# Optimization experiments

Measured on AMD Instinct MI355X. Metric: run time of the kernel, lower is better.

The kernel has to match this reference:

```python
import jax, jax.numpy as jnp
import numpy as np

# ---- Cl(4,1) Cayley table (signature [1,1,1,1,-1]), basis blades indexed by 5-bit mask ----
_METRIC = np.array([1, 1, 1, 1, -1], dtype=np.float32)

def _build_gp_map():
    T = np.zeros((32, 32, 32), dtype=np.float32)
    for a in range(32):
        for b in range(32):
            # canonical reordering sign (count generator swaps)
            s, aa = 0, a >> 1
            while aa:
                s += bin(aa & b).count('1')
                aa >>= 1
            sign = -1.0 if (s & 1) else 1.0
            # metric contribution of annihilated common generators
            common = a & b
            for i in range(5):
                if (common >> i) & 1:
                    sign *= _METRIC[i]
            T[a, b, a ^ b] = sign  # e_a * e_b = sign * e_{a XOR b}
    return T

GP_MAP = _build_gp_map()  # [32, 32, 32], one signed nonzero per (a,b) pair

IN_FEATURES = 256
OUT_FEATURES = 256
BATCH, SEQ = 4, 512


def setup_inputs() -> dict:
    key = jax.random.key(0)
    kx, kw = jax.random.split(key)
    x = jax.random.normal(kx, (BATCH, SEQ, IN_FEATURES, 32), dtype=jnp.float32)
    # Versor init: std = sqrt(2 / (fan_in * 32))
    std = (2.0 / (IN_FEATURES * 32)) ** 0.5
    weight = jax.random.normal(kw, (OUT_FEATURES, IN_FEATURES, 32), dtype=jnp.float32) * std
    return {"x": x, "weight": weight}


def normalize_cl41(out, eps=1e-6):
    # Normalize each output multivector by its Euclidean norm over the 32 basis coeffs.
    norm = jnp.sqrt(jnp.sum(out * out, axis=-1, keepdims=True) + eps)
    return out / norm


def reference(x, weight):
    gp = jnp.asarray(GP_MAP, dtype=x.dtype)  # [j, l, k]
    # W_op[o,i,l,k] = sum_j weight[o,i,j] * gp[j,l,k]
    W_op = jnp.einsum('oij,jlk->oilk', weight, gp)
    # out[b,s,o,k] = sum_{i,l} x[b,s,i,l] * W_op[o,i,l,k]
    out = jnp.einsum('bsil,oilk->bsok', x, W_op)
    return normalize_cl41(out)
```

## Files before the change

### kernel.cpp

```cpp
#include <hip/hip_runtime.h>
#include <stdint.h>

#define AS1 __attribute__((address_space(1)))
#define AS3 __attribute__((address_space(3)))

typedef __attribute__((ext_vector_type(8))) short bf16x8;
typedef __attribute__((ext_vector_type(4))) float f32x4;


struct Mono { int col[4]; int ph[4]; };

constexpr Mono mono_mul(Mono A, Mono B) {
    Mono R{};
    for (int r = 0; r < 4; ++r) {
        int k = A.col[r];
        R.col[r] = B.col[k];
        R.ph[r] = (A.ph[r] + B.ph[k]) & 3;
    }
    return R;
}

constexpr Mono gen(int g) {
    Mono E{};
    for (int r = 0; r < 4; ++r) {
        int r1 = (r >> 1) & 1, r0 = r & 1;
        if (g == 0)      { E.col[r] = r ^ 2; E.ph[r] = 0; }
        else if (g == 1) { E.col[r] = r ^ 2; E.ph[r] = r1 ? 1 : 3; }
        else if (g == 2) { E.col[r] = r ^ 1; E.ph[r] = r1 ? 2 : 0; }
        else if (g == 3) { E.col[r] = r ^ 1; E.ph[r] = ((r1 ? 2 : 0) + (r0 ? 1 : 3)) & 3; }
        else             { E.col[r] = r;     E.ph[r] = (1 + (r1 ? 2 : 0) + (r0 ? 2 : 0)) & 3; }
    }
    return E;
}

struct Blades { Mono m[32]; };
constexpr Blades make_blades() {
    Blades B{};
    for (int A = 0; A < 32; ++A) {
        Mono M{};
        for (int r = 0; r < 4; ++r) { M.col[r] = r; M.ph[r] = 0; }
        for (int g = 0; g < 5; ++g)
            if ((A >> g) & 1) M = mono_mul(M, gen(g));
        B.m[A] = M;
    }
    return B;
}
constexpr Blades BL = make_blades();

struct FwdTab { int bl[4][4][2][4]; float sg[4][4][2][4]; };
constexpr FwdTab make_fwd() {
    FwdTab T{};
    int cnt[4][4][2] = {};
    for (int A = 0; A < 32; ++A)
        for (int r = 0; r < 4; ++r) {
            int c = BL.m[A].col[r], p = BL.m[A].ph[r];
            int rc = p & 1;
            int& n = cnt[r][c][rc];
            T.bl[r][c][rc][n] = A;
            T.sg[r][c][rc][n] = (p & 2) ? -1.f : 1.f;
            ++n;
        }
    return T;
}
constexpr FwdTab FT = make_fwd();

__device__ inline unsigned short f2bf(float f) {
    uint32_t u = __float_as_uint(f);
    u += 0x7FFFu + ((u >> 16) & 1u);
    return (unsigned short)(u >> 16);
}

__global__ __launch_bounds__(256) void xform_kernel(const float* __restrict__ x,
                                                    const float* __restrict__ w,
                                                    unsigned short* __restrict__ Xb,
                                                    unsigned short* __restrict__ Wr) {
    if (blockIdx.x < 2048) {
        int t = blockIdx.x * 256 + threadIdx.x;
        int i = t & 255, n = t >> 8;
        float v[32];
        const float4* xp = (const float4*)(x + (size_t)t * 32);
#pragma unroll
        for (int q = 0; q < 8; ++q) {
            float4 f = xp[q];
            v[q * 4 + 0] = f.x; v[q * 4 + 1] = f.y; v[q * 4 + 2] = f.z; v[q * 4 + 3] = f.w;
        }
#pragma unroll
        for (int b = 0; b < 4; ++b) {
            union { unsigned short s[8]; uint4 u; } r;
#pragma unroll
            for (int c = 0; c < 4; ++c)
#pragma unroll
                for (int rc = 0; rc < 2; ++rc) {
                    float s = 0.f;
#pragma unroll
                    for (int j = 0; j < 4; ++j)
                        s += FT.sg[c][b][rc][j] * v[FT.bl[c][b][rc][j]];
                    r.s[c * 2 + rc] = f2bf(s);
                }
            *((uint4*)(Xb + (size_t)(n * 4 + b) * 2048 + i * 8)) = r.u;
        }
    } else {
        int t = (blockIdx.x - 2048) * 256 + threadIdx.x;
        int i = t & 255, o = t >> 8;
        float v[32];
        const float4* wp = (const float4*)(w + (size_t)t * 32);
#pragma unroll
        for (int q = 0; q < 8; ++q) {
            float4 f = wp[q];
            v[q * 4 + 0] = f.x; v[q * 4 + 1] = f.y; v[q * 4 + 2] = f.z; v[q * 4 + 3] = f.w;
        }
        float Re[4][4], Im[4][4];
#pragma unroll
        for (int a = 0; a < 4; ++a)
#pragma unroll
            for (int c = 0; c < 4; ++c) {
                float sr = 0.f, si = 0.f;
#pragma unroll
                for (int j = 0; j < 4; ++j) {
                    sr += FT.sg[a][c][0][j] * v[FT.bl[a][c][0][j]];
                    si += FT.sg[a][c][1][j] * v[FT.bl[a][c][1][j]];
                }
                Re[a][c] = sr; Im[a][c] = si;
            }
#pragma unroll
        for (int ra = 0; ra < 2; ++ra)
#pragma unroll
            for (int a = 0; a < 4; ++a) {
                int m = o * 8 + ra * 4 + a;
                union { unsigned short s[8]; uint4 u; } r;
#pragma unroll
                for (int c = 0; c < 4; ++c) {
                    float v0 = ra == 0 ? Re[a][c] : Im[a][c];
                    float v1 = ra == 0 ? -Im[a][c] : Re[a][c];
                    r.s[c * 2 + 0] = f2bf(v0);
                    r.s[c * 2 + 1] = f2bf(v1);
                }
                *((uint4*)(Wr + (size_t)m * 2048 + i * 8)) = r.u;
            }
    }
}

__global__ __launch_bounds__(256) void gemm_kernel(const unsigned short* __restrict__ A,
                                                   const unsigned short* __restrict__ B,
                                                   float* __restrict__ out) {
    const int K = 2048;
    __shared__ alignas(16) unsigned short SMEM[2 * 128 * 32];
    unsigned short* As = SMEM;
    unsigned short* Bs = SMEM + 128 * 32;
    float* scr = (float*)SMEM;

    int tid = threadIdx.x;
    int wid = tid >> 6, lane = tid & 63;
    int row0 = blockIdx.y * 128;
    int col0 = blockIdx.x * 128;
    int wr = (wid >> 1) * 64, wc = (wid & 1) * 64;
    int lm = lane & 15, quad = lane >> 4;

    f32x4 acc[4][4];
#pragma unroll
    for (int ti = 0; ti < 4; ++ti)
#pragma unroll
        for (int tj = 0; tj < 4; ++tj)
            acc[ti][tj] = (f32x4){0.f, 0.f, 0.f, 0.f};

    for (int k0 = 0; k0 < K; k0 += 32) {
#pragma unroll
        for (int p = 0; p < 2; ++p) {
            int c = p * 256 + tid;
            int m = c >> 2;
            int off = (c & 3) * 8;
            const unsigned short* ga = A + (size_t)(row0 + m) * K + k0 + off;
            const unsigned short* gb = B + (size_t)(col0 + m) * K + k0 + off;
            unsigned short* la = &As[(size_t)(p * 256 + wid * 64) * 8];
            unsigned short* lb = &Bs[(size_t)(p * 256 + wid * 64) * 8];
            __builtin_amdgcn_global_load_lds((const AS1 void*)ga, (AS3 void*)la, 16, 0, 0);
            __builtin_amdgcn_global_load_lds((const AS1 void*)gb, (AS3 void*)lb, 16, 0, 0);
        }
        __syncthreads();

        bf16x8 af[4], bfr[4];
#pragma unroll
        for (int ti = 0; ti < 4; ++ti)
            af[ti] = *(const bf16x8*)&As[(wr + ti * 16 + lm) * 32 + quad * 8];
#pragma unroll
        for (int tj = 0; tj < 4; ++tj)
            bfr[tj] = *(const bf16x8*)&Bs[(wc + tj * 16 + lm) * 32 + quad * 8];
#pragma unroll
        for (int ti = 0; ti < 4; ++ti)
#pragma unroll
            for (int tj = 0; tj < 4; ++tj)
                acc[ti][tj] = __builtin_amdgcn_mfma_f32_16x16x32_bf16(af[ti], bfr[tj],
                                                                      acc[ti][tj], 0, 0, 0);
        __syncthreads();
    }

    int band = wr >> 6;
#pragma unroll
    for (int ti = 0; ti < 4; ++ti) {
        __syncthreads();
#pragma unroll
        for (int tj = 0; tj < 4; ++tj)
#pragma unroll
            for (int r = 0; r < 4; ++r)
                scr[(band * 16 + quad * 4 + r) * 128 + (wc + tj * 16 + lm)] = acc[ti][tj][r];
        __syncthreads();

        if (tid < 128) {
            int n_l = tid & 31, og = tid >> 5;
            int o_local = (og >> 1) * 8 + ti * 2 + (og & 1);
            int srow0 = (og >> 1) * 16 + (og & 1) * 8;
            float V[32];
#pragma unroll
            for (int u = 0; u < 8; ++u) {
                float4 f = *(const float4*)&scr[(srow0 + u) * 128 + n_l * 4];
                int vi = (u >> 2) * 16 + (u & 3) * 4;
                V[vi + 0] = f.x; V[vi + 1] = f.y; V[vi + 2] = f.z; V[vi + 3] = f.w;
            }
            float xa[32];
            float ss = 0.f;
#pragma unroll
            for (int Ab = 0; Ab < 32; ++Ab) {
                float s = 0.f;
#pragma unroll
                for (int a = 0; a < 4; ++a) {
                    const int c = BL.m[Ab].col[a];
                    const int p = BL.m[Ab].ph[a];
                    float vv = V[(p & 1) * 16 + a * 4 + c];
                    s += (p & 2) ? -vv : vv;
                }
                s *= 0.25f;
                xa[Ab] = s;
                ss += s * s;
            }
            float inv = rsqrtf(ss + 1e-6f);
            int n = (col0 >> 2) + n_l;
            int o = (row0 >> 3) + o_local;
            float4* op = (float4*)(out + ((size_t)n * 256 + o) * 32);
#pragma unroll
            for (int q = 0; q < 8; ++q) {
                float4 f;
                f.x = xa[q * 4 + 0] * inv; f.y = xa[q * 4 + 1] * inv;
                f.z = xa[q * 4 + 2] * inv; f.w = xa[q * 4 + 3] * inv;
                op[q] = f;
            }
        }
    }
}

extern "C" void kernel_launch(void* const* d_in, const int* in_sizes, int n_in,
                              void* d_out, int out_size, void* d_ws, size_t ws_size,
                              hipStream_t stream) {
    const float* x = (const float*)d_in[0];
    const float* w = (const float*)d_in[1];
    float* out = (float*)d_out;

    unsigned short* Wr = (unsigned short*)d_ws;
    unsigned short* Xb = (unsigned short*)((char*)d_ws + 8388608);

    hipLaunchKernelGGL(xform_kernel, dim3(2304),   dim3(256), 0, stream, x, w, Xb, Wr);
    hipLaunchKernelGGL(gemm_kernel,  dim3(64, 16), dim3(256), 0, stream, Wr, Xb, out);
}
```

Baseline: 233.0 us.

## Rewrite GEMM with 256x256 tiles, 4-stage LDS pipeline, and swizzled LDS

Reworks the bf16 MFMA GEMM. It now uses 512-thread blocks computing 256x256 tiles, and a four-buffer LDS ring fed by global_load_lds with three tiles in flight, synchronized by explicit vmcnt waits and barriers. This replaces the previous load, sync, compute, sync loop. It also XOR-swizzles the LDS layout to avoid bank conflicts, raises wave priority around the MFMA bursts, and has each wave run the Clifford epilogue and normalization on its own scratch region, removing the block-wide epilogue barriers. The costs are 128KB of LDS, which limits occupancy, and heavy accumulator register pressure; the grid shrinks to 256 blocks.

```diff
diff --git a/kernel.cpp b/kernel.cpp
--- a/kernel.cpp
+++ b/kernel.cpp
@@ -140,110 +140,141 @@
     }
 }
 
-__global__ __launch_bounds__(256) void gemm_kernel(const unsigned short* __restrict__ A,
-                                                   const unsigned short* __restrict__ B,
-                                                   float* __restrict__ out) {
+__global__ __launch_bounds__(512, 2) void gemm_kernel(const unsigned short* __restrict__ A,
+                                                      const unsigned short* __restrict__ B,
+                                                      float* __restrict__ out) {
     const int K = 2048;
-    __shared__ alignas(16) unsigned short SMEM[2 * 128 * 32];
-    unsigned short* As = SMEM;
-    unsigned short* Bs = SMEM + 128 * 32;
-    float* scr = (float*)SMEM;
-
-    int tid = threadIdx.x;
-    int wid = tid >> 6, lane = tid & 63;
-    int row0 = blockIdx.y * 128;
-    int col0 = blockIdx.x * 128;
-    int wr = (wid >> 1) * 64, wc = (wid & 1) * 64;
-    int lm = lane & 15, quad = lane >> 4;
-
-    f32x4 acc[4][4];
-#pragma unroll
-    for (int ti = 0; ti < 4; ++ti)
-#pragma unroll
-        for (int tj = 0; tj < 4; ++tj)
-            acc[ti][tj] = (f32x4){0.f, 0.f, 0.f, 0.f};
-
-    for (int k0 = 0; k0 < K; k0 += 32) {
+    const int NT = 64;
+    __shared__ alignas(16) unsigned short SM[4 * 16384];
+
+    const int tid = threadIdx.x;
+    const int wid = tid >> 6, lane = tid & 63;
+    const int lm = lane & 15, quad = lane >> 4;
+    const int wm = wid >> 2, wn = wid & 3;
+    const int row0 = blockIdx.y * 256;
+    const int col0 = blockIdx.x * 256;
+
+    size_t gA[2], gB[2];
+    int ldsA[2], ldsB[2];
+#pragma unroll
+    for (int p = 0; p < 2; ++p) {
+        int g = p * 512 + tid;
+        int r = g >> 2, c = g & 3;
+        int sc = c ^ ((r >> 1) & 3);
+        gA[p] = (size_t)(row0 + r) * K + sc * 8;
+        gB[p] = (size_t)(col0 + r) * K + sc * 8;
+        ldsA[p] = (p * 512 + wid * 64) * 8;
+        ldsB[p] = 8192 + (p * 512 + wid * 64) * 8;
+    }
+
+    const int swz = (lm >> 1) & 3;
+    const int aoff = (wm * 128 + lm) * 32 + (quad ^ swz) * 8;
+    const int boff = 8192 + (wn * 64 + lm) * 32 + (quad ^ swz) * 8;
+
+    f32x4 acc[8][4];
+#pragma unroll
+    for (int i = 0; i < 8; ++i)
+#pragma unroll
+        for (int j = 0; j < 4; ++j) acc[i][j] = (f32x4){0.f, 0.f, 0.f, 0.f};
+
+    auto ISSUE = [&](int t) {
+        const int bb = (t & 3) * 16384;
+        const int k0 = t * 32;
 #pragma unroll
         for (int p = 0; p < 2; ++p) {
-            int c = p * 256 + tid;
-            int m = c >> 2;
-            int off = (c & 3) * 8;
-            const unsigned short* ga = A + (size_t)(row0 + m) * K + k0 + off;
-            const unsigned short* gb = B + (size_t)(col0 + m) * K + k0 + off;
-            unsigned short* la = &As[(size_t)(p * 256 + wid * 64) * 8];
-            unsigned short* lb = &Bs[(size_t)(p * 256 + wid * 64) * 8];
-            __builtin_amdgcn_global_load_lds((const AS1 void*)ga, (AS3 void*)la, 16, 0, 0);
-            __builtin_amdgcn_global_load_lds((const AS1 void*)gb, (AS3 void*)lb, 16, 0, 0);
-        }
-        __syncthreads();
-
-        bf16x8 af[4], bfr[4];
-#pragma unroll
-        for (int ti = 0; ti < 4; ++ti)
-            af[ti] = *(const bf16x8*)&As[(wr + ti * 16 + lm) * 32 + quad * 8];
-#pragma unroll
-        for (int tj = 0; tj < 4; ++tj)
-            bfr[tj] = *(const bf16x8*)&Bs[(wc + tj * 16 + lm) * 32 + quad * 8];
-#pragma unroll
-        for (int ti = 0; ti < 4; ++ti)
-#pragma unroll
-            for (int tj = 0; tj < 4; ++tj)
-                acc[ti][tj] = __builtin_amdgcn_mfma_f32_16x16x32_bf16(af[ti], bfr[tj],
-                                                                      acc[ti][tj], 0, 0, 0);
-        __syncthreads();
-    }
-
-    int band = wr >> 6;
-#pragma unroll
-    for (int ti = 0; ti < 4; ++ti) {
-        __syncthreads();
-#pragma unroll
-        for (int tj = 0; tj < 4; ++tj)
-#pragma unroll
-            for (int r = 0; r < 4; ++r)
-                scr[(band * 16 + quad * 4 + r) * 128 + (wc + tj * 16 + lm)] = acc[ti][tj][r];
-        __syncthreads();
-
-        if (tid < 128) {
-            int n_l = tid & 31, og = tid >> 5;
-            int o_local = (og >> 1) * 8 + ti * 2 + (og & 1);
-            int srow0 = (og >> 1) * 16 + (og & 1) * 8;
-            float V[32];
-#pragma unroll
-            for (int u = 0; u < 8; ++u) {
-                float4 f = *(const float4*)&scr[(srow0 + u) * 128 + n_l * 4];
-                int vi = (u >> 2) * 16 + (u & 3) * 4;
-                V[vi + 0] = f.x; V[vi + 1] = f.y; V[vi + 2] = f.z; V[vi + 3] = f.w;
+            __builtin_amdgcn_global_load_lds((const AS1 void*)(A + gA[p] + k0),
+                                             (AS3 void*)(&SM[bb + ldsA[p]]), 16, 0, 0);
+            __builtin_amdgcn_global_load_lds((const AS1 void*)(B + gB[p] + k0),
+                                             (AS3 void*)(&SM[bb + ldsB[p]]), 16, 0, 0);
+        }
+    };
+    auto COMPUTE = [&](int t) {
+        const int bb = (t & 3) * 16384;
+        bf16x8 av[8], bv[4];
+#pragma unroll
+        for (int fn = 0; fn < 4; ++fn) bv[fn] = *(const bf16x8*)&SM[bb + boff + fn * 512];
+#pragma unroll
+        for (int fm = 0; fm < 8; ++fm) av[fm] = *(const bf16x8*)&SM[bb + aoff + fm * 512];
+        __builtin_amdgcn_s_setprio(1);
+#pragma unroll
+        for (int fm = 0; fm < 8; ++fm)
+#pragma unroll
+            for (int fn = 0; fn < 4; ++fn)
+                acc[fm][fn] = __builtin_amdgcn_mfma_f32_16x16x32_bf16(av[fm], bv[fn],
+                                                                      acc[fm][fn], 0, 0, 0);
+        __builtin_amdgcn_s_setprio(0);
+    };
+
+    ISSUE(0); ISSUE(1); ISSUE(2);
+    for (int t = 0; t < NT - 3; ++t) {
+        asm volatile("s_waitcnt vmcnt(8)" ::: "memory");
+        __builtin_amdgcn_s_barrier();
+        ISSUE(t + 3);
+        COMPUTE(t);
+    }
+    asm volatile("s_waitcnt vmcnt(8)" ::: "memory");
+    __builtin_amdgcn_s_barrier();
+    COMPUTE(NT - 3);
+    asm volatile("s_waitcnt vmcnt(4)" ::: "memory");
+    __builtin_amdgcn_s_barrier();
+    COMPUTE(NT - 2);
+    asm volatile("s_waitcnt vmcnt(0)" ::: "memory");
+    __builtin_amdgcn_s_barrier();
+    COMPUTE(NT - 1);
+    __syncthreads();
+
+    float* scrw = (float*)SM + wid * 2048;
+    const int nl = lane >> 2, ol = lane & 3;
+#pragma unroll
+    for (int s = 0; s < 4; ++s) {
+#pragma unroll
+        for (int h = 0; h < 2; ++h)
+#pragma unroll
+            for (int fn = 0; fn < 4; ++fn)
+#pragma unroll
+                for (int r = 0; r < 4; ++r) {
+                    int rw = h * 16 + quad * 4 + r;
+                    int cc = (fn * 16 + lm) ^ (quad << 3);
+                    scrw[rw * 64 + cc] = acc[s * 2 + h][fn][r];
+                }
+        asm volatile("s_waitcnt lgkmcnt(0)" ::: "memory");
+        float V[32];
+#pragma unroll
+        for (int u = 0; u < 8; ++u) {
+            int row = ol * 8 + u;
+            int cb = (nl * 4) ^ (((row >> 2) & 3) << 3);
+            float4 f = *(const float4*)&scrw[row * 64 + cb];
+            int vi = (u >> 2) * 16 + (u & 3) * 4;
+            V[vi + 0] = f.x; V[vi + 1] = f.y; V[vi + 2] = f.z; V[vi + 3] = f.w;
+        }
+        float xa[32];
+        float ss = 0.f;
+#pragma unroll
+        for (int Ab = 0; Ab < 32; ++Ab) {
+            float sv = 0.f;
+#pragma unroll
+            for (int a = 0; a < 4; ++a) {
+                const int c = BL.m[Ab].col[a];
+                const int p = BL.m[Ab].ph[a];
+                float vv = V[(p & 1) * 16 + a * 4 + c];
+                sv += (p & 2) ? -vv : vv;
             }
-            float xa[32];
-            float ss = 0.f;
-#pragma unroll
-            for (int Ab = 0; Ab < 32; ++Ab) {
-                float s = 0.f;
-#pragma unroll
-                for (int a = 0; a < 4; ++a) {
-                    const int c = BL.m[Ab].col[a];
-                    const int p = BL.m[Ab].ph[a];
-                    float vv = V[(p & 1) * 16 + a * 4 + c];
-                    s += (p & 2) ? -vv : vv;
-                }
-                s *= 0.25f;
-                xa[Ab] = s;
-                ss += s * s;
-            }
-            float inv = rsqrtf(ss + 1e-6f);
-            int n = (col0 >> 2) + n_l;
-            int o = (row0 >> 3) + o_local;
-            float4* op = (float4*)(out + ((size_t)n * 256 + o) * 32);
-#pragma unroll
-            for (int q = 0; q < 8; ++q) {
-                float4 f;
-                f.x = xa[q * 4 + 0] * inv; f.y = xa[q * 4 + 1] * inv;
-                f.z = xa[q * 4 + 2] * inv; f.w = xa[q * 4 + 3] * inv;
-                op[q] = f;
-            }
-        }
+            sv *= 0.25f;
+            xa[Ab] = sv;
+            ss += sv * sv;
+        }
+        float inv = rsqrtf(ss + 1e-6f);
+        int o = (row0 >> 3) + wm * 16 + s * 4 + ol;
+        int n = (col0 >> 2) + wn * 16 + nl;
+        float4* op = (float4*)(out + ((size_t)n * 256 + o) * 32);
+#pragma unroll
+        for (int q = 0; q < 8; ++q) {
+            float4 f;
+            f.x = xa[q * 4 + 0] * inv; f.y = xa[q * 4 + 1] * inv;
+            f.z = xa[q * 4 + 2] * inv; f.w = xa[q * 4 + 3] * inv;
+            op[q] = f;
+        }
+        asm volatile("s_waitcnt lgkmcnt(0)" ::: "memory");
     }
 }
 
@@ -257,6 +288,6 @@
     unsigned short* Wr = (unsigned short*)d_ws;
     unsigned short* Xb = (unsigned short*)((char*)d_ws + 8388608);
 
-    hipLaunchKernelGGL(xform_kernel, dim3(2304),   dim3(256), 0, stream, x, w, Xb, Wr);
-    hipLaunchKernelGGL(gemm_kernel,  dim3(64, 16), dim3(256), 0, stream, Wr, Xb, out);
-}
+    hipLaunchKernelGGL(xform_kernel, dim3(2304),  dim3(256), 0, stream, x, w, Xb, Wr);
+    hipLaunchKernelGGL(gemm_kernel,  dim3(32, 8), dim3(512), 0, stream, Wr, Xb, out);
+}
```

New measurement: 194.0 us. 1.2x faster.
